# Kernel optimization log

Measured on AMD Instinct MI355X. Metric: run time of the kernel, lower is better.

The kernel has to match this reference:

```python
import jax, jax.numpy as jnp
import numpy as np

B, C, H, W = 4, 64, 160, 160
K = 3
KK = K * K
PAD = (K - 1) // 2
EPS = 1e-5


def conv2d(x, w, b):
    y = jax.lax.conv_general_dilated(
        x, w, (1, 1), [(PAD, PAD), (PAD, PAD)],
        dimension_numbers=('NCHW', 'OIHW', 'NCHW'))
    return y + b[None, :, None, None]


def batchnorm(x, g, b, m, v):
    # eval-mode BN with running stats
    return (x - m[None, :, None, None]) * jax.lax.rsqrt(v + EPS)[None, :, None, None] * g[None, :, None, None] + b[None, :, None, None]


def bilinear_gather(x, py, px):
    # x: [B,C,H,W]; py,px: [B,KK,H,W] float sample coords -> [B,C,KK,H,W]
    Bx, Cx, Hx, Wx = x.shape
    y0 = jnp.floor(py)
    x0 = jnp.floor(px)
    ly = py - y0
    lx = px - x0
    x_flat = x.reshape(Bx, Cx, 1, Hx * Wx)
    acc = jnp.zeros((Bx, Cx, py.shape[1], Hx * Wx), dtype=x.dtype)
    corners = ((y0, x0, (1 - ly) * (1 - lx)),
               (y0, x0 + 1, (1 - ly) * lx),
               (y0 + 1, x0, ly * (1 - lx)),
               (y0 + 1, x0 + 1, ly * lx))
    for yi, xi, wgt in corners:
        valid = (yi >= 0) & (yi < Hx) & (xi >= 0) & (xi < Wx)
        yc = jnp.clip(yi, 0, Hx - 1).astype(jnp.int32)
        xc = jnp.clip(xi, 0, Wx - 1).astype(jnp.int32)
        idx = (yc * Wx + xc).reshape(Bx, -1, Hx * Wx)          # [B,KK,HW]
        g = jnp.take_along_axis(x_flat, idx[:, None], axis=3)  # [B,C,KK,HW]
        acc = acc + (wgt * valid).reshape(Bx, 1, -1, Hx * Wx) * g
    return acc.reshape(Bx, Cx, -1, Hx, Wx)


def modulated_deform_conv(x, offset, mask, weight):
    # x:[B,C,H,W] offset:[B,2*KK,H,W] (mmcv layout: pairs (dy,dx) interleaved) mask:[B,KK,H,W]
    Bx, Cx, Hx, Wx = x.shape
    Co = weight.shape[0]
    off = offset.reshape(Bx, KK, 2, Hx, Wx)
    k = jnp.arange(KK)
    ki = (k // K).astype(x.dtype)
    kj = (k % K).astype(x.dtype)
    ys = jnp.arange(Hx, dtype=x.dtype)
    xs = jnp.arange(Wx, dtype=x.dtype)
    py = ys[None, None, :, None] - PAD + ki[None, :, None, None] + off[:, :, 0]
    px = xs[None, None, None, :] - PAD + kj[None, :, None, None] + off[:, :, 1]
    samp = bilinear_gather(x, py, px)            # [B,C,KK,H,W]
    samp = samp * mask[:, None]                  # modulation
    return jnp.einsum('bckhw,ock->bohw', samp, weight.reshape(Co, Cx, KK))


def setup_inputs() -> dict:
    key = jax.random.key(0)
    ks = jax.random.split(key, 16)
    inp = {
        'x': jax.random.normal(ks[0], (B, C, H, W), jnp.float32),
        'w_om1': jax.random.normal(ks[1], (3 * KK, C, K, K), jnp.float32) * 0.01,
        'b_om1': jax.random.normal(ks[2], (3 * KK,), jnp.float32) * 0.01,
        'w_dcn1': jax.random.normal(ks[3], (C, C, K, K), jnp.float32) * 0.04,
        'bn1_g': jax.random.uniform(ks[4], (C,), jnp.float32, 0.5, 1.5),
        'bn1_b': jax.random.normal(ks[5], (C,), jnp.float32) * 0.1,
        'bn1_m': jax.random.normal(ks[6], (C,), jnp.float32) * 0.1,
        'bn1_v': jax.random.uniform(ks[7], (C,), jnp.float32, 0.5, 1.5),
        'w_om2': jax.random.normal(ks[8], (3 * KK, C, K, K), jnp.float32) * 0.01,
        'b_om2': jax.random.normal(ks[9], (3 * KK,), jnp.float32) * 0.01,
        'w_dcn2': jax.random.normal(ks[10], (C, C, K, K), jnp.float32) * 0.04,
        'bn2_g': jax.random.uniform(ks[11], (C,), jnp.float32, 0.5, 1.5),
        'bn2_b': jax.random.normal(ks[12], (C,), jnp.float32) * 0.1,
        'bn2_m': jax.random.normal(ks[13], (C,), jnp.float32) * 0.1,
        'bn2_v': jax.random.uniform(ks[14], (C,), jnp.float32, 0.5, 1.5),
    }
    return inp


def reference(x, w_om1, b_om1, w_dcn1, bn1_g, bn1_b, bn1_m, bn1_v,
              w_om2, b_om2, w_dcn2, bn2_g, bn2_b, bn2_m, bn2_v):
    identity = x
    om1 = conv2d(x, w_om1, b_om1)
    o1, o2, m1 = jnp.split(om1, 3, axis=1)
    offset1 = jnp.concatenate([o1, o2], axis=1)
    mask1 = jax.nn.sigmoid(m1)
    out = modulated_deform_conv(x, offset1, mask1, w_dcn1)
    out = batchnorm(out, bn1_g, bn1_b, bn1_m, bn1_v)
    out = jax.nn.gelu(out, approximate=False)
    om2 = conv2d(out, w_om2, b_om2)
    o1b, o2b, m2 = jnp.split(om2, 3, axis=1)
    offset2 = jnp.concatenate([o1b, o2b], axis=1)
    mask2 = jax.nn.sigmoid(m2)
    out = modulated_deform_conv(out, offset2, mask2, w_dcn2)
    out = batchnorm(out, bn2_g, bn2_b, bn2_m, bn2_v)
    out = out + identity
    return jax.nn.gelu(out, approximate=False)
```

## Files before the change

kernel.cpp:

```cpp
#include <hip/hip_runtime.h>
#include <math.h>

#define HH 160
#define WW 160
#define HWSZ 25600
#define TR 14
#define TC 22
#define NSLOT 308

typedef __attribute__((ext_vector_type(8))) short short8;
typedef __attribute__((ext_vector_type(4))) short short4v;
typedef __attribute__((ext_vector_type(8))) _Float16 half8;
typedef __attribute__((ext_vector_type(2))) _Float16 half2v;
typedef __attribute__((ext_vector_type(4))) float f32x4;

__device__ __forceinline__ short f2h(float f) {
  union { _Float16 h; short s; } u; u.h = (_Float16)f; return u.s;
}
__device__ __forceinline__ float h2f(short s) {
  union { _Float16 h; short s; } u; u.s = s; return (float)u.h;
}
__device__ __forceinline__ half2v bcast_h(short s) {
  unsigned int x = (unsigned short)s; x |= x << 16;
  union { unsigned int u; half2v h; } v; v.u = x; return v.h;
}

__global__ __launch_bounds__(256) void pre_kernel(
    const float* __restrict__ x,
    const float* __restrict__ g1, const float* __restrict__ b1,
    const float* __restrict__ m1, const float* __restrict__ v1,
    const float* __restrict__ g2, const float* __restrict__ b2,
    const float* __restrict__ m2, const float* __restrict__ v2,
    const float* __restrict__ wd1, const float* __restrict__ wd2,
    const float* __restrict__ wo1, const float* __restrict__ wo2,
    float* __restrict__ sc, short* __restrict__ wd1h, short* __restrict__ wd2h,
    short* __restrict__ wo1h, short* __restrict__ wo2h,
    short* __restrict__ xcl) {
  __shared__ short tmp[64][72];
  int t = threadIdx.x;
  int bx = blockIdx.x;
  if (bx < 1600) {
    int b = bx / 400, p0 = (bx - b * 400) * 64;
    const float* xb = x + (size_t)b * 64 * HWSZ;
    for (int i = t; i < 4096; i += 256) {
      int c = i >> 6, p = i & 63;
      tmp[p][c] = f2h(xb[c * HWSZ + p0 + p]);
    }
    __syncthreads();
    short* ob = xcl + ((size_t)b * HWSZ + p0) * 64;
    for (int i = t; i < 512; i += 256) {
      int p = i >> 3, g = i & 7;
      *(short8*)&ob[p * 64 + g * 8] = *(const short8*)&tmp[p][g * 8];
    }
    return;
  }
  int i0 = (bx - 1600) * 256 + t;
  for (int i = i0; i < 36864; i += 16384) {
    int j = i & 7, m = (i >> 3) & 15, q = (i >> 7) & 3;
    int ot = (i >> 9) & 3, f = i >> 11;
    int kp = f * 32 + q * 8 + j;
    int k = kp >> 6, c = kp & 63;
    int src = (ot * 16 + m) * 576 + c * 9 + k;
    wd1h[i] = f2h(wd1[src]);
    wd2h[i] = f2h(wd2[src]);
  }
  for (int i = i0; i < 18432; i += 16384) {
    int j = i & 7, q = (i >> 3) & 3, m = (i >> 5) & 15;
    int ot = (i >> 9) & 1, f = i >> 10;
    int kp = f * 32 + q * 8 + j;
    int k = kp >> 6, c = kp & 63;
    int oc = ot * 16 + m;
    wo1h[i] = (oc < 27) ? f2h(wo1[oc * 576 + c * 9 + k]) : (short)0;
    wo2h[i] = (oc < 27) ? f2h(wo2[oc * 576 + c * 9 + k]) : (short)0;
  }
  if (i0 < 64) {
    float s1 = g1[i0] * rsqrtf(v1[i0] + 1e-5f);
    sc[i0]       = s1;
    sc[64 + i0]  = b1[i0] - m1[i0] * s1;
    float s2 = g2[i0] * rsqrtf(v2[i0] + 1e-5f);
    sc[128 + i0] = s2;
    sc[192 + i0] = b2[i0] - m2[i0] * s2;
  }
}

__global__ __launch_bounds__(512, 6) void dcn_fused(
    const short* __restrict__ xcl,
    const short* __restrict__ who,
    const float* __restrict__ bias_om,
    const short* __restrict__ whd,
    const float* __restrict__ scale, const float* __restrict__ shift,
    const short* __restrict__ id_cl,
    short* __restrict__ out_cl,
    float* __restrict__ out_f32) {
  __shared__ short xt[NSLOT * 64];
  __shared__ __align__(16) short As[4608];

  int t = threadIdx.x;
  int x0 = blockIdx.x * 16, y0 = blockIdx.y * 8, b = blockIdx.z;
  int w = t >> 6, lane = t & 63, q = lane >> 4, m = lane & 15;
  int ybase = y0 - 3, xbase = x0 - 3;

  short8 pr = *(const short8*)&whd[t * 8];

  const short* xb = xcl + (size_t)b * HWSZ * 64;
  for (int i = t; i < NSLOT * 8; i += 512) {
    int slot = i >> 3, g = i & 7;
    int ty = slot / TC, tx = slot - ty * TC;
    int gy = ybase + ty, gx = xbase + tx;
    short8 v = {};
    if (gy >= 0 && gy < HH && gx >= 0 && gx < WW)
      v = *(const short8*)&xb[(gy * WW + gx) * 64 + g * 8];
    *(short8*)&xt[slot * 64 + ((g ^ (slot & 7)) << 3)] = v;
  }
  __syncthreads();

  {
    f32x4 oacc0 = {}, oacc1 = {};
#pragma unroll 6
    for (int f = 0; f < 18; f++) {
      int k = f >> 1;
      int ki = k / 3, kj = k - ki * 3;
      int g = (f & 1) * 4 + q;
      int slotb = (w + ki + 2) * TC + (m + kj + 2);
      short8 bv = *(const short8*)&xt[slotb * 64 + ((g ^ (slotb & 7)) << 3)];
      const short* ap = who + (f * 128 + m * 4 + q) * 8;
      short8 a0 = *(const short8*)ap;
      short8 a1 = *(const short8*)(ap + 512);
      union { short8 s8; half8 h; } A0, A1, B;
      A0.s8 = a0; A1.s8 = a1; B.s8 = bv;
      oacc0 = __builtin_amdgcn_mfma_f32_16x16x32_f16(A0.h, B.h, oacc0, 0, 0, 0);
      oacc1 = __builtin_amdgcn_mfma_f32_16x16x32_f16(A1.h, B.h, oacc1, 0, 0, 0);
    }
    int px = w * 16 + m;
#pragma unroll
    for (int mt = 0; mt < 2; mt++) {
      f32x4 oa = mt ? oacc1 : oacc0;
      short4v pv;
#pragma unroll
      for (int r = 0; r < 4; r++) {
        int oc = mt * 16 + q * 4 + r;
        float bb = (oc < 27) ? bias_om[oc] : 0.f;
        pv[r] = f2h(oa[r] + bb);
      }
      *(short4v*)&As[px * 36 + mt * 16 + q * 4] = pv;
    }
  }
  __syncthreads();

  union { short s[36]; short4v v4[9]; } omr;
  {
    int px = w * 16 + m;
#pragma unroll
    for (int i = 0; i < 9; i++)
      omr.v4[i] = *(const short4v*)&As[px * 36 + i * 4];
  }

  f32x4 acc[4] = {};
#pragma unroll
  for (int k = 0; k < 9; k++) {
    __syncthreads();
    *(short8*)&As[t * 8] = pr;
    if (k < 8)
      pr = *(const short8*)&whd[(k + 1) * 4096 + t * 8];
    __syncthreads();

    int y = y0 + w, x = x0 + m;
    float dy = h2f(omr.s[2 * k]);
    float dx = h2f(omr.s[2 * k + 1]);
    float ml = h2f(omr.s[18 + k]);
    float msk = 1.f / (1.f + __expf(-ml));
    int ki = k / 3, kj = k - ki * 3;
    float py  = (float)(y - 1 + ki) + dy;
    float pxf = (float)(x - 1 + kj) + dx;
    float fy = floorf(py), fx = floorf(pxf);
    float ly = py - fy, lx = pxf - fx;
    int yi0 = (int)fy, xi0 = (int)fx;
    bool vy0 = (yi0 >= 0) & (yi0 < HH), vy1 = (yi0 + 1 >= 0) & (yi0 + 1 < HH);
    bool vx0 = (xi0 >= 0) & (xi0 < WW), vx1 = (xi0 + 1 >= 0) & (xi0 + 1 < WW);
    int ty0 = min(max(yi0 - ybase, 0), TR - 2);
    int tx0 = min(max(xi0 - xbase, 0), TC - 2);
    int p00 = ty0 * TC + tx0;
    half2v w00 = bcast_h(f2h((vy0 & vx0) ? (1.f - ly) * (1.f - lx) * msk : 0.f));
    half2v w01 = bcast_h(f2h((vy0 & vx1) ? (1.f - ly) * lx * msk : 0.f));
    half2v w10 = bcast_h(f2h((vy1 & vx0) ? ly * (1.f - lx) * msk : 0.f));
    half2v w11 = bcast_h(f2h((vy1 & vx1) ? ly * lx * msk : 0.f));
    int s00 = p00, s01 = p00 + 1, s10 = p00 + TC, s11 = p00 + TC + 1;
#pragma unroll
    for (int ch = 0; ch < 2; ch++) {
      int g = ch * 4 + q;
      const short* ap = As + ch * 2048 + (q * 16 + m) * 8;
      short8 a0 = *(const short8*)ap;
      short8 a1 = *(const short8*)(ap + 512);
      short8 a2 = *(const short8*)(ap + 1024);
      short8 a3 = *(const short8*)(ap + 1536);
      union { short8 s8; half2v h[4]; } c00, c01, c10, c11, bb;
      c00.s8 = *(const short8*)&xt[s00 * 64 + ((g ^ (s00 & 7)) << 3)];
      c01.s8 = *(const short8*)&xt[s01 * 64 + ((g ^ (s01 & 7)) << 3)];
      c10.s8 = *(const short8*)&xt[s10 * 64 + ((g ^ (s10 & 7)) << 3)];
      c11.s8 = *(const short8*)&xt[s11 * 64 + ((g ^ (s11 & 7)) << 3)];
#pragma unroll
      for (int d = 0; d < 4; d++)
        bb.h[d] = c00.h[d] * w00 + c01.h[d] * w01 + c10.h[d] * w10 +
                  c11.h[d] * w11;
      union { short8 s8; half8 h8; } B, A0, A1, A2, A3;
      B.s8 = bb.s8; A0.s8 = a0; A1.s8 = a1; A2.s8 = a2; A3.s8 = a3;
      acc[0] = __builtin_amdgcn_mfma_f32_16x16x32_f16(A0.h8, B.h8, acc[0], 0, 0, 0);
      acc[1] = __builtin_amdgcn_mfma_f32_16x16x32_f16(A1.h8, B.h8, acc[1], 0, 0, 0);
      acc[2] = __builtin_amdgcn_mfma_f32_16x16x32_f16(A2.h8, B.h8, acc[2], 0, 0, 0);
      acc[3] = __builtin_amdgcn_mfma_f32_16x16x32_f16(A3.h8, B.h8, acc[3], 0, 0, 0);
    }
  }

  int y = y0 + w, x = x0 + m;
  if (out_f32) {
    size_t pbase = ((size_t)b * HWSZ + y * WW + x) * 64;
#pragma unroll
    for (int ot = 0; ot < 4; ot++) {
      short4v iv = *(const short4v*)&id_cl[pbase + ot * 16 + q * 4];
#pragma unroll
      for (int r = 0; r < 4; r++) {
        int oc = ot * 16 + q * 4 + r;
        size_t idx = ((size_t)(b * 64 + oc)) * HWSZ + y * WW + x;
        float v = acc[ot][r] * scale[oc] + shift[oc] + h2f(iv[r]);
        v = 0.5f * v * (1.f + erff(v * 0.70710678118654752f));
        out_f32[idx] = v;
      }
    }
  } else {
    size_t base = ((size_t)b * HWSZ + y * WW + x) * 64;
#pragma unroll
    for (int ot = 0; ot < 4; ot++) {
      short4v pv;
#pragma unroll
      for (int r = 0; r < 4; r++) {
        int oc = ot * 16 + q * 4 + r;
        float v = acc[ot][r] * scale[oc] + shift[oc];
        v = 0.5f * v * (1.f + erff(v * 0.70710678118654752f));
        pv[r] = f2h(v);
      }
      *(short4v*)&out_cl[base + ot * 16 + q * 4] = pv;
    }
  }
}

extern "C" void kernel_launch(void* const* d_in, const int* in_sizes, int n_in,
                              void* d_out, int out_size, void* d_ws, size_t ws_size,
                              hipStream_t stream) {
  const float* x     = (const float*)d_in[0];
  const float* w_om1 = (const float*)d_in[1];
  const float* b_om1 = (const float*)d_in[2];
  const float* w_d1  = (const float*)d_in[3];
  const float* bn1g  = (const float*)d_in[4];
  const float* bn1b  = (const float*)d_in[5];
  const float* bn1m  = (const float*)d_in[6];
  const float* bn1v  = (const float*)d_in[7];
  const float* w_om2 = (const float*)d_in[8];
  const float* b_om2 = (const float*)d_in[9];
  const float* w_d2  = (const float*)d_in[10];
  const float* bn2g  = (const float*)d_in[11];
  const float* bn2b  = (const float*)d_in[12];
  const float* bn2m  = (const float*)d_in[13];
  const float* bn2v  = (const float*)d_in[14];

  float* ws    = (float*)d_ws;
  float* sc    = ws;
  short* w1h   = (short*)(ws + 256);
  short* w2h   = w1h + 36864;
  short* wo1h  = w2h + 36864;
  short* wo2h  = wo1h + 18432;
  short* x_cl  = (short*)(ws + 55552);
  short* o1_cl = x_cl + 6553600;
  float* outp  = (float*)d_out;

  pre_kernel<<<dim3(1664), dim3(256), 0, stream>>>(
      x, bn1g, bn1b, bn1m, bn1v, bn2g, bn2b, bn2m, bn2v,
      w_d1, w_d2, w_om1, w_om2, sc, w1h, w2h, wo1h, wo2h, x_cl);

  dim3 grid(WW / 16, HH / 8, 4);
  dcn_fused<<<grid, dim3(512), 0, stream>>>(
      x_cl, wo1h, b_om1, w1h, sc, sc + 64, nullptr, o1_cl, nullptr);
  dcn_fused<<<grid, dim3(512), 0, stream>>>(
      o1_cl, wo2h, b_om2, w2h, sc + 128, sc + 192, x_cl, nullptr, outp);
}
```

Baseline: 207.8 us.

## Switch deform-conv GEMM to 32x32x16 MFMA with 256-thread blocks and 3-tap weight staging

Blocks shrink from 512 to 256 threads. The deformable GEMM now uses 32x32x16 MFMA over 32 pixels per wave, and the weight layout is repacked to match. Weights are staged into LDS three taps at a time, so there are 3 barrier pairs instead of 9, and identity loads are hoisted ahead of the main loop. The offset conv now has each wave cover two rows. This trades more registers and LDS per block, and lower occupancy, for fewer barriers and bigger MFMA tiles.

Result: no change. 209.0 us (+0.6%).

```diff
diff --git a/kernel.cpp b/kernel.cpp
--- a/kernel.cpp
+++ b/kernel.cpp
@@ -13,6 +13,7 @@
 typedef __attribute__((ext_vector_type(8))) _Float16 half8;
 typedef __attribute__((ext_vector_type(2))) _Float16 half2v;
 typedef __attribute__((ext_vector_type(4))) float f32x4;
+typedef __attribute__((ext_vector_type(16))) float f32x16;
 
 __device__ __forceinline__ short f2h(float f) {
   union { _Float16 h; short s; } u; u.h = (_Float16)f; return u.s;
@@ -56,11 +57,9 @@
   }
   int i0 = (bx - 1600) * 256 + t;
   for (int i = i0; i < 36864; i += 16384) {
-    int j = i & 7, m = (i >> 3) & 15, q = (i >> 7) & 3;
-    int ot = (i >> 9) & 3, f = i >> 11;
-    int kp = f * 32 + q * 8 + j;
-    int k = kp >> 6, c = kp & 63;
-    int src = (ot * 16 + m) * 576 + c * 9 + k;
+    int j = i & 7, oc = (i >> 3) & 31, hi = (i >> 8) & 1;
+    int ot = (i >> 9) & 1, s = (i >> 10) & 3, tap = i >> 12;
+    int src = (ot * 32 + oc) * 576 + (s * 16 + hi * 8 + j) * 9 + tap;
     wd1h[i] = f2h(wd1[src]);
     wd2h[i] = f2h(wd2[src]);
   }
@@ -83,7 +82,7 @@
   }
 }
 
-__global__ __launch_bounds__(512, 6) void dcn_fused(
+__global__ __launch_bounds__(256, 2) void dcn_fused(
     const short* __restrict__ xcl,
     const short* __restrict__ who,
     const float* __restrict__ bias_om,
@@ -93,17 +92,22 @@
     short* __restrict__ out_cl,
     float* __restrict__ out_f32) {
   __shared__ short xt[NSLOT * 64];
-  __shared__ __align__(16) short As[4608];
+  __shared__ __align__(16) short wA[12288];
+  __shared__ __align__(16) short oms[4608];
 
   int t = threadIdx.x;
   int x0 = blockIdx.x * 16, y0 = blockIdx.y * 8, b = blockIdx.z;
   int w = t >> 6, lane = t & 63, q = lane >> 4, m = lane & 15;
+  int hi = lane >> 5, p31 = lane & 31;
   int ybase = y0 - 3, xbase = x0 - 3;
 
-  short8 pr = *(const short8*)&whd[t * 8];
+  short8 pr[6];
+#pragma unroll
+  for (int c = 0; c < 6; c++)
+    pr[c] = *(const short8*)&whd[c * 2048 + t * 8];
 
   const short* xb = xcl + (size_t)b * HWSZ * 64;
-  for (int i = t; i < NSLOT * 8; i += 512) {
+  for (int i = t; i < NSLOT * 8; i += 256) {
     int slot = i >> 3, g = i & 7;
     int ty = slot / TC, tx = slot - ty * TC;
     int gy = ybase + ty, gx = xbase + tx;
@@ -112,116 +116,144 @@
       v = *(const short8*)&xb[(gy * WW + gx) * 64 + g * 8];
     *(short8*)&xt[slot * 64 + ((g ^ (slot & 7)) << 3)] = v;
   }
+#pragma unroll
+  for (int c = 0; c < 6; c++)
+    *(short8*)&wA[c * 2048 + t * 8] = pr[c];
+#pragma unroll
+  for (int c = 0; c < 6; c++)
+    pr[c] = *(const short8*)&whd[12288 + c * 2048 + t * 8];
   __syncthreads();
 
   {
-    f32x4 oacc0 = {}, oacc1 = {};
+    f32x4 oacc[2][2] = {};
 #pragma unroll 6
     for (int f = 0; f < 18; f++) {
       int k = f >> 1;
       int ki = k / 3, kj = k - ki * 3;
       int g = (f & 1) * 4 + q;
-      int slotb = (w + ki + 2) * TC + (m + kj + 2);
-      short8 bv = *(const short8*)&xt[slotb * 64 + ((g ^ (slotb & 7)) << 3)];
       const short* ap = who + (f * 128 + m * 4 + q) * 8;
       short8 a0 = *(const short8*)ap;
       short8 a1 = *(const short8*)(ap + 512);
-      union { short8 s8; half8 h; } A0, A1, B;
-      A0.s8 = a0; A1.s8 = a1; B.s8 = bv;
-      oacc0 = __builtin_amdgcn_mfma_f32_16x16x32_f16(A0.h, B.h, oacc0, 0, 0, 0);
-      oacc1 = __builtin_amdgcn_mfma_f32_16x16x32_f16(A1.h, B.h, oacc1, 0, 0, 0);
-    }
-    int px = w * 16 + m;
-#pragma unroll
-    for (int mt = 0; mt < 2; mt++) {
-      f32x4 oa = mt ? oacc1 : oacc0;
-      short4v pv;
-#pragma unroll
-      for (int r = 0; r < 4; r++) {
-        int oc = mt * 16 + q * 4 + r;
-        float bb = (oc < 27) ? bias_om[oc] : 0.f;
-        pv[r] = f2h(oa[r] + bb);
-      }
-      *(short4v*)&As[px * 36 + mt * 16 + q * 4] = pv;
+      union { short8 s8; half8 h; } A0, A1;
+      A0.s8 = a0; A1.s8 = a1;
+#pragma unroll
+      for (int p = 0; p < 2; p++) {
+        int slotb = (w * 2 + p + ki + 2) * TC + (m + kj + 2);
+        union { short8 s8; half8 h; } B;
+        B.s8 = *(const short8*)&xt[slotb * 64 + ((g ^ (slotb & 7)) << 3)];
+        oacc[p][0] = __builtin_amdgcn_mfma_f32_16x16x32_f16(A0.h, B.h, oacc[p][0], 0, 0, 0);
+        oacc[p][1] = __builtin_amdgcn_mfma_f32_16x16x32_f16(A1.h, B.h, oacc[p][1], 0, 0, 0);
+      }
+    }
+#pragma unroll
+    for (int p = 0; p < 2; p++) {
+      int px = w * 32 + p * 16 + m;
+#pragma unroll
+      for (int mt = 0; mt < 2; mt++) {
+        short4v pv;
+#pragma unroll
+        for (int r = 0; r < 4; r++) {
+          int oc = mt * 16 + q * 4 + r;
+          float bb = (oc < 27) ? bias_om[oc] : 0.f;
+          pv[r] = f2h(oacc[p][mt][r] + bb);
+        }
+        *(short4v*)&oms[px * 36 + mt * 16 + q * 4] = pv;
+      }
     }
   }
   __syncthreads();
 
   union { short s[36]; short4v v4[9]; } omr;
   {
-    int px = w * 16 + m;
+    int px = w * 32 + p31;
 #pragma unroll
     for (int i = 0; i < 9; i++)
-      omr.v4[i] = *(const short4v*)&As[px * 36 + i * 4];
-  }
-
-  f32x4 acc[4] = {};
-#pragma unroll
-  for (int k = 0; k < 9; k++) {
-    __syncthreads();
-    *(short8*)&As[t * 8] = pr;
-    if (k < 8)
-      pr = *(const short8*)&whd[(k + 1) * 4096 + t * 8];
-    __syncthreads();
-
-    int y = y0 + w, x = x0 + m;
-    float dy = h2f(omr.s[2 * k]);
-    float dx = h2f(omr.s[2 * k + 1]);
-    float ml = h2f(omr.s[18 + k]);
-    float msk = 1.f / (1.f + __expf(-ml));
-    int ki = k / 3, kj = k - ki * 3;
-    float py  = (float)(y - 1 + ki) + dy;
-    float pxf = (float)(x - 1 + kj) + dx;
-    float fy = floorf(py), fx = floorf(pxf);
-    float ly = py - fy, lx = pxf - fx;
-    int yi0 = (int)fy, xi0 = (int)fx;
-    bool vy0 = (yi0 >= 0) & (yi0 < HH), vy1 = (yi0 + 1 >= 0) & (yi0 + 1 < HH);
-    bool vx0 = (xi0 >= 0) & (xi0 < WW), vx1 = (xi0 + 1 >= 0) & (xi0 + 1 < WW);
-    int ty0 = min(max(yi0 - ybase, 0), TR - 2);
-    int tx0 = min(max(xi0 - xbase, 0), TC - 2);
-    int p00 = ty0 * TC + tx0;
-    half2v w00 = bcast_h(f2h((vy0 & vx0) ? (1.f - ly) * (1.f - lx) * msk : 0.f));
-    half2v w01 = bcast_h(f2h((vy0 & vx1) ? (1.f - ly) * lx * msk : 0.f));
-    half2v w10 = bcast_h(f2h((vy1 & vx0) ? ly * (1.f - lx) * msk : 0.f));
-    half2v w11 = bcast_h(f2h((vy1 & vx1) ? ly * lx * msk : 0.f));
-    int s00 = p00, s01 = p00 + 1, s10 = p00 + TC, s11 = p00 + TC + 1;
-#pragma unroll
-    for (int ch = 0; ch < 2; ch++) {
-      int g = ch * 4 + q;
-      const short* ap = As + ch * 2048 + (q * 16 + m) * 8;
-      short8 a0 = *(const short8*)ap;
-      short8 a1 = *(const short8*)(ap + 512);
-      short8 a2 = *(const short8*)(ap + 1024);
-      short8 a3 = *(const short8*)(ap + 1536);
-      union { short8 s8; half2v h[4]; } c00, c01, c10, c11, bb;
-      c00.s8 = *(const short8*)&xt[s00 * 64 + ((g ^ (s00 & 7)) << 3)];
-      c01.s8 = *(const short8*)&xt[s01 * 64 + ((g ^ (s01 & 7)) << 3)];
-      c10.s8 = *(const short8*)&xt[s10 * 64 + ((g ^ (s10 & 7)) << 3)];
-      c11.s8 = *(const short8*)&xt[s11 * 64 + ((g ^ (s11 & 7)) << 3)];
-#pragma unroll
-      for (int d = 0; d < 4; d++)
-        bb.h[d] = c00.h[d] * w00 + c01.h[d] * w01 + c10.h[d] * w10 +
-                  c11.h[d] * w11;
-      union { short8 s8; half8 h8; } B, A0, A1, A2, A3;
-      B.s8 = bb.s8; A0.s8 = a0; A1.s8 = a1; A2.s8 = a2; A3.s8 = a3;
-      acc[0] = __builtin_amdgcn_mfma_f32_16x16x32_f16(A0.h8, B.h8, acc[0], 0, 0, 0);
-      acc[1] = __builtin_amdgcn_mfma_f32_16x16x32_f16(A1.h8, B.h8, acc[1], 0, 0, 0);
-      acc[2] = __builtin_amdgcn_mfma_f32_16x16x32_f16(A2.h8, B.h8, acc[2], 0, 0, 0);
-      acc[3] = __builtin_amdgcn_mfma_f32_16x16x32_f16(A3.h8, B.h8, acc[3], 0, 0, 0);
-    }
-  }
-
-  int y = y0 + w, x = x0 + m;
+      omr.v4[i] = *(const short4v*)&oms[px * 36 + i * 4];
+  }
+
+  int y = y0 + w * 2 + (p31 >> 4), x = x0 + m;
+
+  short4v ivs[8];
   if (out_f32) {
     size_t pbase = ((size_t)b * HWSZ + y * WW + x) * 64;
 #pragma unroll
-    for (int ot = 0; ot < 4; ot++) {
-      short4v iv = *(const short4v*)&id_cl[pbase + ot * 16 + q * 4];
-#pragma unroll
-      for (int r = 0; r < 4; r++) {
-        int oc = ot * 16 + q * 4 + r;
+    for (int ot = 0; ot < 2; ot++)
+#pragma unroll
+      for (int blk = 0; blk < 4; blk++)
+        ivs[ot * 4 + blk] =
+            *(const short4v*)&id_cl[pbase + ot * 32 + blk * 8 + hi * 4];
+  }
+
+  f32x16 acc0 = {}, acc1 = {};
+#pragma unroll
+  for (int grp = 0; grp < 3; ++grp) {
+    if (grp > 0) {
+      __syncthreads();
+#pragma unroll
+      for (int c = 0; c < 6; c++)
+        *(short8*)&wA[c * 2048 + t * 8] = pr[c];
+      if (grp < 2) {
+#pragma unroll
+        for (int c = 0; c < 6; c++)
+          pr[c] = *(const short8*)&whd[(grp + 1) * 12288 + c * 2048 + t * 8];
+      }
+      __syncthreads();
+    }
+#pragma unroll
+    for (int kt = 0; kt < 3; ++kt) {
+      const int k = grp * 3 + kt;
+      float dy = h2f(omr.s[2 * k]);
+      float dx = h2f(omr.s[2 * k + 1]);
+      float ml = h2f(omr.s[18 + k]);
+      float msk = 1.f / (1.f + __expf(-ml));
+      int ki = k / 3, kj = k - ki * 3;
+      float py  = (float)(y - 1 + ki) + dy;
+      float pxf = (float)(x - 1 + kj) + dx;
+      float fy = floorf(py), fx = floorf(pxf);
+      float ly = py - fy, lx = pxf - fx;
+      int yi0 = (int)fy, xi0 = (int)fx;
+      bool vy0 = (yi0 >= 0) & (yi0 < HH), vy1 = (yi0 + 1 >= 0) & (yi0 + 1 < HH);
+      bool vx0 = (xi0 >= 0) & (xi0 < WW), vx1 = (xi0 + 1 >= 0) & (xi0 + 1 < WW);
+      int ty0 = min(max(yi0 - ybase, 0), TR - 2);
+      int tx0 = min(max(xi0 - xbase, 0), TC - 2);
+      int p00 = ty0 * TC + tx0;
+      half2v w00 = bcast_h(f2h((vy0 & vx0) ? (1.f - ly) * (1.f - lx) * msk : 0.f));
+      half2v w01 = bcast_h(f2h((vy0 & vx1) ? (1.f - ly) * lx * msk : 0.f));
+      half2v w10 = bcast_h(f2h((vy1 & vx0) ? ly * (1.f - lx) * msk : 0.f));
+      half2v w11 = bcast_h(f2h((vy1 & vx1) ? ly * lx * msk : 0.f));
+      int s00 = p00, s01 = p00 + 1, s10 = p00 + TC, s11 = p00 + TC + 1;
+#pragma unroll
+      for (int s = 0; s < 4; s++) {
+        int g = s * 2 + hi;
+        union { short8 s8; half2v h[4]; } c00, c01, c10, c11, bb;
+        c00.s8 = *(const short8*)&xt[s00 * 64 + ((g ^ (s00 & 7)) << 3)];
+        c01.s8 = *(const short8*)&xt[s01 * 64 + ((g ^ (s01 & 7)) << 3)];
+        c10.s8 = *(const short8*)&xt[s10 * 64 + ((g ^ (s10 & 7)) << 3)];
+        c11.s8 = *(const short8*)&xt[s11 * 64 + ((g ^ (s11 & 7)) << 3)];
+#pragma unroll
+        for (int d = 0; d < 4; d++)
+          bb.h[d] = c00.h[d] * w00 + c01.h[d] * w01 + c10.h[d] * w10 +
+                    c11.h[d] * w11;
+        const short* ap = wA + kt * 4096 + s * 1024 + lane * 8;
+        short8 a0 = *(const short8*)ap;
+        short8 a1 = *(const short8*)(ap + 512);
+        union { short8 s8; half8 h8; } B, A0, A1;
+        B.s8 = bb.s8; A0.s8 = a0; A1.s8 = a1;
+        acc0 = __builtin_amdgcn_mfma_f32_32x32x16_f16(A0.h8, B.h8, acc0, 0, 0, 0);
+        acc1 = __builtin_amdgcn_mfma_f32_32x32x16_f16(A1.h8, B.h8, acc1, 0, 0, 0);
+      }
+    }
+  }
+
+  if (out_f32) {
+#pragma unroll
+    for (int ot = 0; ot < 2; ot++) {
+#pragma unroll
+      for (int r = 0; r < 16; r++) {
+        int oc = ot * 32 + (r & 3) + 8 * (r >> 2) + 4 * hi;
+        float a = ot ? acc1[r] : acc0[r];
         size_t idx = ((size_t)(b * 64 + oc)) * HWSZ + y * WW + x;
-        float v = acc[ot][r] * scale[oc] + shift[oc] + h2f(iv[r]);
+        float v = a * scale[oc] + shift[oc] + h2f(ivs[ot * 4 + (r >> 2)][r & 3]);
         v = 0.5f * v * (1.f + erff(v * 0.70710678118654752f));
         out_f32[idx] = v;
       }
@@ -229,16 +261,21 @@
   } else {
     size_t base = ((size_t)b * HWSZ + y * WW + x) * 64;
 #pragma unroll
-    for (int ot = 0; ot < 4; ot++) {
-      short4v pv;
-#pragma unroll
-      for (int r = 0; r < 4; r++) {
-        int oc = ot * 16 + q * 4 + r;
-        float v = acc[ot][r] * scale[oc] + shift[oc];
-        v = 0.5f * v * (1.f + erff(v * 0.70710678118654752f));
-        pv[r] = f2h(v);
-      }
-      *(short4v*)&out_cl[base + ot * 16 + q * 4] = pv;
+    for (int ot = 0; ot < 2; ot++) {
+#pragma unroll
+      for (int blk = 0; blk < 4; blk++) {
+        short4v pv;
+#pragma unroll
+        for (int rr = 0; rr < 4; rr++) {
+          int r = blk * 4 + rr;
+          int oc = ot * 32 + blk * 8 + hi * 4 + rr;
+          float a = ot ? acc1[r] : acc0[r];
+          float v = a * scale[oc] + shift[oc];
+          v = 0.5f * v * (1.f + erff(v * 0.70710678118654752f));
+          pv[rr] = f2h(v);
+        }
+        *(short4v*)&out_cl[base + ot * 32 + blk * 8 + hi * 4] = pv;
+      }
     }
   }
 }
@@ -277,8 +314,8 @@
       w_d1, w_d2, w_om1, w_om2, sc, w1h, w2h, wo1h, wo2h, x_cl);
 
   dim3 grid(WW / 16, HH / 8, 4);
-  dcn_fused<<<grid, dim3(512), 0, stream>>>(
+  dcn_fused<<<grid, dim3(256), 0, stream>>>(
       x_cl, wo1h, b_om1, w1h, sc, sc + 64, nullptr, o1_cl, nullptr);
-  dcn_fused<<<grid, dim3(512), 0, stream>>>(
+  dcn_fused<<<grid, dim3(256), 0, stream>>>(
       o1_cl, wo2h, b_om2, w2h, sc + 128, sc + 192, x_cl, nullptr, outp);
 }
```

## Read DCN weights directly from global memory and drop block barriers in main loop

Applied to the files above, without the earlier changes.

Stops staging the deformable-conv weight slices through shared memory with two block barriers per kernel tap. Each wave now loads its MFMA A-operands straight from global (L1/L2-cached) memory, using a reordered weight layout so that lane loads are contiguous. The offset/mask staging buffer shrinks and is synchronised with a wave-level barrier instead of a block barrier, and the identity loads are hoisted ahead of the loop. This removes 18 barriers and the LDS traffic, at the cost of more global/L1 load latency inside the loop.

After: 240.7 us. 15.8% more time.

```diff
diff --git a/kernel.cpp b/kernel.cpp
--- a/kernel.cpp
+++ b/kernel.cpp
@@ -56,7 +56,7 @@
   }
   int i0 = (bx - 1600) * 256 + t;
   for (int i = i0; i < 36864; i += 16384) {
-    int j = i & 7, m = (i >> 3) & 15, q = (i >> 7) & 3;
+    int j = i & 7, q = (i >> 3) & 3, m = (i >> 5) & 15;
     int ot = (i >> 9) & 3, f = i >> 11;
     int kp = f * 32 + q * 8 + j;
     int k = kp >> 6, c = kp & 63;
@@ -93,14 +93,12 @@
     short* __restrict__ out_cl,
     float* __restrict__ out_f32) {
   __shared__ short xt[NSLOT * 64];
-  __shared__ __align__(16) short As[4608];
+  __shared__ __align__(16) short oms[3584];
 
   int t = threadIdx.x;
   int x0 = blockIdx.x * 16, y0 = blockIdx.y * 8, b = blockIdx.z;
   int w = t >> 6, lane = t & 63, q = lane >> 4, m = lane & 15;
   int ybase = y0 - 3, xbase = x0 - 3;
-
-  short8 pr = *(const short8*)&whd[t * 8];
 
   const short* xb = xcl + (size_t)b * HWSZ * 64;
   for (int i = t; i < NSLOT * 8; i += 512) {
@@ -142,29 +140,35 @@
         float bb = (oc < 27) ? bias_om[oc] : 0.f;
         pv[r] = f2h(oa[r] + bb);
       }
-      *(short4v*)&As[px * 36 + mt * 16 + q * 4] = pv;
-    }
-  }
-  __syncthreads();
-
-  union { short s[36]; short4v v4[9]; } omr;
+      if (mt == 0 || q != 3)
+        *(short4v*)&oms[px * 28 + mt * 16 + q * 4] = pv;
+    }
+  }
+
+  asm volatile("s_waitcnt lgkmcnt(0)" ::: "memory");
+  __builtin_amdgcn_wave_barrier();
+
+  union { short s[28]; short4v v4[7]; } omr;
   {
     int px = w * 16 + m;
 #pragma unroll
-    for (int i = 0; i < 9; i++)
-      omr.v4[i] = *(const short4v*)&As[px * 36 + i * 4];
+    for (int i = 0; i < 7; i++)
+      omr.v4[i] = *(const short4v*)&oms[px * 28 + i * 4];
+  }
+
+  int y = y0 + w, x = x0 + m;
+
+  short4v ivs[4];
+  if (out_f32) {
+    size_t pbase = ((size_t)b * HWSZ + y * WW + x) * 64;
+#pragma unroll
+    for (int ot = 0; ot < 4; ot++)
+      ivs[ot] = *(const short4v*)&id_cl[pbase + ot * 16 + q * 4];
   }
 
   f32x4 acc[4] = {};
 #pragma unroll
   for (int k = 0; k < 9; k++) {
-    __syncthreads();
-    *(short8*)&As[t * 8] = pr;
-    if (k < 8)
-      pr = *(const short8*)&whd[(k + 1) * 4096 + t * 8];
-    __syncthreads();
-
-    int y = y0 + w, x = x0 + m;
     float dy = h2f(omr.s[2 * k]);
     float dx = h2f(omr.s[2 * k + 1]);
     float ml = h2f(omr.s[18 + k]);
@@ -188,7 +192,7 @@
 #pragma unroll
     for (int ch = 0; ch < 2; ch++) {
       int g = ch * 4 + q;
-      const short* ap = As + ch * 2048 + (q * 16 + m) * 8;
+      const short* ap = whd + (2 * k + ch) * 2048 + m * 32 + q * 8;
       short8 a0 = *(const short8*)ap;
       short8 a1 = *(const short8*)(ap + 512);
       short8 a2 = *(const short8*)(ap + 1024);
@@ -211,17 +215,14 @@
     }
   }
 
-  int y = y0 + w, x = x0 + m;
   if (out_f32) {
-    size_t pbase = ((size_t)b * HWSZ + y * WW + x) * 64;
 #pragma unroll
     for (int ot = 0; ot < 4; ot++) {
-      short4v iv = *(const short4v*)&id_cl[pbase + ot * 16 + q * 4];
 #pragma unroll
       for (int r = 0; r < 4; r++) {
         int oc = ot * 16 + q * 4 + r;
         size_t idx = ((size_t)(b * 64 + oc)) * HWSZ + y * WW + x;
-        float v = acc[ot][r] * scale[oc] + shift[oc] + h2f(iv[r]);
+        float v = acc[ot][r] * scale[oc] + shift[oc] + h2f(ivs[ot][r]);
         v = 0.5f * v * (1.f + erff(v * 0.70710678118654752f));
         out_f32[idx] = v;
       }
```
